# Performance work log

Measured on AMD Instinct MI355X. Metric: run time of the kernel, lower is better.

Reference implementation:

```python
import jax, jax.numpy as jnp
import numpy as np

SEQ = 4096
BLOCK = 64            # sparse_block_size
BLOCKS = SEQ // BLOCK # 64 block rows/cols
NUM_ORACLES = 32
ORACLE = SEQ // NUM_ORACLES      # 128
LOCAL_BLOCKS = ORACLE // BLOCK   # 2 (sliding-window width in blocks)
PATTERN_ID = 0


def _build_block_mask(pattern_id=PATTERN_ID):
    # Mirrors DKernelPredefinedSparseAttention.__init__ create_mask((i,))
    q_pos = np.arange(BLOCKS)[:, None]
    k_pos = np.arange(BLOCKS)[None, :]
    causal = q_pos >= k_pos
    sliding = (q_pos - k_pos) < LOCAL_BLOCKS
    vert = np.zeros(BLOCKS, dtype=bool)
    real_col = int(pattern_id * ORACLE + 0.5)
    cs = real_col // BLOCK
    ce = (real_col + ORACLE) // BLOCK
    vert[cs:ce] = True
    vert[0:1] = True  # global block 0 always visible
    return causal & (sliding | vert[None, :])


def setup_inputs() -> dict:
    key = jax.random.key(0)
    kq, kk, kv = jax.random.split(key, 3)
    shape = (1, SEQ, 8, 128)  # bshd, matches module's own smoke test layout
    q = jax.random.normal(kq, shape, dtype=jnp.float32)
    k = jax.random.normal(kk, shape, dtype=jnp.float32)
    v = jax.random.normal(kv, shape, dtype=jnp.float32)
    block_mask = jnp.asarray(_build_block_mask())  # [BLOCKS, BLOCKS] bool
    return {"q": q, "k": k, "v": v, "block_mask": block_mask}


def reference(q, k, v, block_mask):
    # Expand block-level mask to token level: [S, S]
    tok_mask = jnp.repeat(jnp.repeat(block_mask, BLOCK, axis=0), BLOCK, axis=1)
    scale = 1.0 / jnp.sqrt(jnp.asarray(q.shape[-1], q.dtype))
    # bshd x bshd -> bhqk scores
    scores = jnp.einsum("bqhd,bkhd->bhqk", q, k) * scale
    neg = jnp.asarray(-1e30, scores.dtype)
    scores = jnp.where(tok_mask[None, None, :, :], scores, neg)
    probs = jax.nn.softmax(scores, axis=-1)
    out = jnp.einsum("bhqk,bkhd->bqhd", probs, v)
    return out
```

## Files before the change

### kernel.cpp

```cpp
#include <hip/hip_runtime.h>
#include <hip/hip_bf16.h>

typedef __bf16 bf16x4 __attribute__((ext_vector_type(4)));
typedef __bf16 bf16x8 __attribute__((ext_vector_type(8)));
typedef short short4v __attribute__((ext_vector_type(4)));
typedef float floatx4 __attribute__((ext_vector_type(4)));

constexpr int SEQ = 4096;
constexpr int NH  = 8;
constexpr int DH  = 128;
constexpr int BLK = 64;
constexpr int QBLOCKS = SEQ / BLK;
constexpr int RS = NH * DH;
constexpr float SCALE = 0.088388347648318447f;
constexpr float MSHIFT = 8.0f;

#if __has_builtin(__builtin_amdgcn_mfma_f32_16x16x16_bf16)
  #define HAVE_PV16 1
  __device__ __forceinline__ floatx4 pv16(bf16x4 a, bf16x4 b, floatx4 c) {
      return __builtin_amdgcn_mfma_f32_16x16x16_bf16(a, b, c, 0, 0, 0);
  }
#elif __has_builtin(__builtin_amdgcn_mfma_f32_16x16x16bf16_1k)
  #define HAVE_PV16 1
  __device__ __forceinline__ floatx4 pv16(bf16x4 a, bf16x4 b, floatx4 c) {
      short4v as, bs;
      __builtin_memcpy(&as, &a, 8);
      __builtin_memcpy(&bs, &b, 8);
      return __builtin_amdgcn_mfma_f32_16x16x16bf16_1k(as, bs, c, 0, 0, 0);
  }
#else
  #define HAVE_PV16 0
#endif

__device__ __forceinline__ int calc_blist(int qb, int* blist) {
    int cand[4] = {0, 1, qb - 1, qb};
    int nb = 0;
    for (int i = 0; i < 4; ++i) {
        int b = cand[i];
        if (b < 0 || b > qb) continue;
        bool dup = false;
        for (int j = 0; j < nb; ++j) dup = dup || (blist[j] == b);
        if (!dup) blist[nb++] = b;
    }
    return nb;
}

__device__ __forceinline__ bf16x8 load8f(const float* p) {
    float4 a = *(const float4*)p;
    float4 b = *(const float4*)(p + 4);
    bf16x8 r = { (__bf16)a.x, (__bf16)a.y, (__bf16)a.z, (__bf16)a.w,
                 (__bf16)b.x, (__bf16)b.y, (__bf16)b.z, (__bf16)b.w };
    return r;
}

__global__ __launch_bounds__(1024, 4) void sparse_attn_kernel(
    const float* __restrict__ Q,
    const float* __restrict__ K,
    const float* __restrict__ V,
    float* __restrict__ Out)
{
    const int qb   = blockIdx.x;
    const int h    = blockIdx.y;
    const int tid  = threadIdx.x;
    const int wave = tid >> 6;
    const int g    = wave >> 2;
    const int ws   = wave & 3;
    const int lane = tid & 63;
    const int quad = lane >> 4;
    const int l16  = lane & 15;

    __shared__ __align__(16) __bf16 smem[4 * 8192];
    __bf16* vq    = smem + g * 8192;
    float*  l_arr = (float*)smem;

    int blist[4];
    const int nb = calc_blist(qb, blist);
    const bool valid = (g < nb);
    const int kb = valid ? blist[g] : 0;

    const int qrow = qb * BLK + ws * 16 + l16;
    const float* qp = Q + (size_t)qrow * RS + h * DH;
    bf16x8 qfrag[4];
#pragma unroll
    for (int sx = 0; sx < 4; ++sx)
        qfrag[sx] = load8f(qp + sx * 32 + quad * 8);

    const int tg   = tid & 255;
    const int dh   = tg & 127;
    const int kq   = tg >> 7;
    const int dht  = dh >> 4;
    const int l16v = dh & 15;
    if (valid) {
        const float* base = V + (size_t)(kb * BLK + kq * 32) * RS + h * DH + dh;
#if HAVE_PV16
#pragma unroll
        for (int n2 = 0; n2 < 2; ++n2) {
            const int n = kq * 2 + n2;
#pragma unroll
            for (int qv = 0; qv < 4; ++qv) {
                bf16x4 pk;
#pragma unroll
                for (int j = 0; j < 4; ++j)
                    pk[j] = (__bf16)base[(size_t)(n2 * 16 + qv * 4 + j) * RS];
                *(bf16x4*)(vq + ((n * 8 + dht) * 64 + qv * 16 + l16v) * 4) = pk;
            }
        }
#else
#pragma unroll
        for (int qv = 0; qv < 4; ++qv) {
            bf16x8 pk;
#pragma unroll
            for (int j = 0; j < 8; ++j)
                pk[j] = (__bf16)base[(size_t)(qv * 8 + j) * RS];
            *(bf16x8*)(vq + ((kq * 8 + dht) * 64 + qv * 16 + l16v) * 8) = pk;
        }
#endif
    }

    floatx4 sfragT[4];
    float lp = 0.f;
    if (valid) {
#pragma unroll
        for (int n = 0; n < 4; ++n) {
            floatx4 c = floatx4{0.f, 0.f, 0.f, 0.f};
            const float* kp =
                K + (size_t)(kb * BLK + n * 16 + l16) * RS + h * DH;
#pragma unroll
            for (int sx = 0; sx < 4; ++sx) {
                bf16x8 kf = load8f(kp + sx * 32 + quad * 8);
                c = __builtin_amdgcn_mfma_f32_16x16x32_bf16(kf, qfrag[sx], c, 0, 0, 0);
            }
            sfragT[n] = c;
        }
#pragma unroll
        for (int n = 0; n < 4; ++n)
#pragma unroll
            for (int r = 0; r < 4; ++r) {
                float p = __expf(fmaf(sfragT[n][r], SCALE, -MSHIFT));
                sfragT[n][r] = p;
                lp += p;
            }
        lp += __shfl_xor(lp, 16, 64);
        lp += __shfl_xor(lp, 32, 64);
    }

    __syncthreads();

    floatx4 o_acc[8];
#pragma unroll
    for (int n = 0; n < 8; ++n) o_acc[n] = floatx4{0.f, 0.f, 0.f, 0.f};
    if (valid) {
#if HAVE_PV16
        bf16x4 pa[4];
#pragma unroll
        for (int n = 0; n < 4; ++n) {
            bf16x4 t = { (__bf16)sfragT[n][0], (__bf16)sfragT[n][1],
                         (__bf16)sfragT[n][2], (__bf16)sfragT[n][3] };
            pa[n] = t;
        }
#pragma unroll
        for (int d = 0; d < 8; ++d)
#pragma unroll
            for (int n = 0; n < 4; ++n) {
                bf16x4 vb = *(const bf16x4*)(vq + ((n * 8 + d) * 64 + lane) * 4);
                o_acc[d] = pv16(pa[n], vb, o_acc[d]);
            }
#else
        bf16x8 pa8[2];
#pragma unroll
        for (int s2 = 0; s2 < 2; ++s2) {
            bf16x8 t;
#pragma unroll
            for (int jj = 0; jj < 8; ++jj) {
                const int srcl = ((quad & 1) * 2 + (jj >> 2)) * 16 + l16;
                float a = __shfl(sfragT[2 * s2][jj & 3], srcl, 64);
                float b = __shfl(sfragT[2 * s2 + 1][jj & 3], srcl, 64);
                t[jj] = (__bf16)((quad >> 1) ? b : a);
            }
            pa8[s2] = t;
        }
#pragma unroll
        for (int d = 0; d < 8; ++d)
#pragma unroll
            for (int s2 = 0; s2 < 2; ++s2) {
                bf16x8 vb = *(const bf16x8*)(vq + ((s2 * 8 + d) * 64 + lane) * 8);
                o_acc[d] = __builtin_amdgcn_mfma_f32_16x16x32_bf16(pa8[s2], vb, o_acc[d], 0, 0, 0);
            }
#endif
    }

    __syncthreads();

    if (valid) {
        if (g > 0) {
#pragma unroll
            for (int r = 0; r < 4; ++r) {
                const int row = ws * 16 + quad * 4 + r;
                bf16x8 w;
#pragma unroll
                for (int d = 0; d < 8; ++d) w[d] = (__bf16)o_acc[d][r];
                *(bf16x8*)(vq + row * 128 + l16 * 8) = w;
            }
        }
        if (quad == 0) l_arr[g * 64 + ws * 16 + l16] = lp;
    }
    __syncthreads();

    if (g == 0) {
#pragma unroll
        for (int r = 0; r < 4; ++r) {
            const int row = ws * 16 + quad * 4 + r;
            float l_tot = __shfl(lp, quad * 4 + r, 64);
            float os[8];
#pragma unroll
            for (int d = 0; d < 8; ++d) os[d] = o_acc[d][r];
            for (int gg = 1; gg < nb; ++gg) {
                l_tot += l_arr[gg * 64 + row];
                bf16x8 w = *(const bf16x8*)(smem + gg * 8192 + row * 128 + l16 * 8);
#pragma unroll
                for (int d = 0; d < 8; ++d) os[d] += (float)w[d];
            }
            const float inv = 1.f / l_tot;
            float* op = Out + (size_t)(qb * BLK + row) * RS + h * DH + l16;
#pragma unroll
            for (int d = 0; d < 8; ++d)
                op[d * 16] = os[d] * inv;
        }
    }
}

extern "C" void kernel_launch(void* const* d_in, const int* in_sizes, int n_in,
                              void* d_out, int out_size, void* d_ws, size_t ws_size,
                              hipStream_t stream) {
    const float* Q = (const float*)d_in[0];
    const float* K = (const float*)d_in[1];
    const float* V = (const float*)d_in[2];
    float* Out = (float*)d_out;

    dim3 grid(QBLOCKS, NH);
    sparse_attn_kernel<<<grid, 1024, 0, stream>>>(Q, K, V, Out);
}
```

Measured before the change: 141.9 us.

## Pre-pack Q/K/V to bf16 MFMA-friendly layout in a separate kernel

Adds a pack kernel that converts Q, K and V from fp32 to bf16 once, storing Q/K head-major and V pre-swizzled into the MFMA B-operand layout in workspace. The attention kernel then reads bf16 fragments straight from global memory, with no per-block fp32 conversion, no V staging through shared memory and one fewer barrier. Each K/V block is read by several query blocks, so converting once avoids redundant fp32 loads and conversions. The cost is a second kernel launch plus a round trip of the packed tensors through workspace memory.

```diff
diff --git a/kernel.cpp b/kernel.cpp
--- a/kernel.cpp
+++ b/kernel.cpp
@@ -14,6 +14,9 @@
 constexpr int RS = NH * DH;
 constexpr float SCALE = 0.088388347648318447f;
 constexpr float MSHIFT = 8.0f;
+
+constexpr size_t KP_OFF = (size_t)NH * SEQ * DH * 2;
+constexpr size_t VP_OFF = 2 * KP_OFF;
 
 #if __has_builtin(__builtin_amdgcn_mfma_f32_16x16x16_bf16)
   #define HAVE_PV16 1
@@ -53,10 +56,66 @@
     return r;
 }
 
-__global__ __launch_bounds__(1024, 4) void sparse_attn_kernel(
+__global__ __launch_bounds__(256) void pack_kernel(
     const float* __restrict__ Q,
     const float* __restrict__ K,
     const float* __restrict__ V,
+    __bf16* __restrict__ Qp,
+    __bf16* __restrict__ Kp,
+    __bf16* __restrict__ Vp)
+{
+    const int qb  = blockIdx.x;
+    const int h   = blockIdx.y;
+    const int z   = blockIdx.z;
+    const int tid = threadIdx.x;
+
+    if (z < 2) {
+        const float* src = (z == 0) ? Q : K;
+        __bf16* dst = (z == 0) ? Qp : Kp;
+        const int row = tid >> 2;
+        const int d0  = (tid & 3) * 32;
+        const float* ip = src + (size_t)(qb * BLK + row) * RS + h * DH + d0;
+        __bf16* op = dst + (size_t)(h * SEQ + qb * BLK + row) * DH + d0;
+#pragma unroll
+        for (int c = 0; c < 4; ++c)
+            *(bf16x8*)(op + c * 8) = load8f(ip + c * 8);
+    } else {
+        const int dh   = tid & 127;
+        const int kq   = tid >> 7;
+        const int dht  = dh >> 4;
+        const int l16v = dh & 15;
+        const float* base = V + (size_t)(qb * BLK + kq * 32) * RS + h * DH + dh;
+        __bf16* vt = Vp + (size_t)(h * QBLOCKS + qb) * 8192;
+#if HAVE_PV16
+#pragma unroll
+        for (int n2 = 0; n2 < 2; ++n2) {
+            const int n = kq * 2 + n2;
+#pragma unroll
+            for (int qv = 0; qv < 4; ++qv) {
+                bf16x4 pk;
+#pragma unroll
+                for (int j = 0; j < 4; ++j)
+                    pk[j] = (__bf16)base[(size_t)(n2 * 16 + qv * 4 + j) * RS];
+                *(bf16x4*)(vt + ((n * 8 + dht) * 64 + qv * 16 + l16v) * 4) = pk;
+            }
+        }
+#else
+#pragma unroll
+        for (int qv = 0; qv < 4; ++qv) {
+            bf16x8 pk;
+#pragma unroll
+            for (int j = 0; j < 8; ++j)
+                pk[j] = (__bf16)base[(size_t)(qv * 8 + j) * RS];
+            *(bf16x8*)(vt + ((kq * 8 + dht) * 64 + qv * 16 + l16v) * 8) = pk;
+        }
+#endif
+    }
+}
+
+__global__ __launch_bounds__(1024, 4) void attn_kernel(
+    const __bf16* __restrict__ Qp,
+    const __bf16* __restrict__ Kp,
+    const __bf16* __restrict__ Vp,
     float* __restrict__ Out)
 {
     const int qb   = blockIdx.x;
@@ -70,7 +129,7 @@
     const int l16  = lane & 15;
 
     __shared__ __align__(16) __bf16 smem[4 * 8192];
-    __bf16* vq    = smem + g * 8192;
+    __bf16* pq    = smem + g * 8192;
     float*  l_arr = (float*)smem;
 
     int blist[4];
@@ -78,44 +137,11 @@
     const bool valid = (g < nb);
     const int kb = valid ? blist[g] : 0;
 
-    const int qrow = qb * BLK + ws * 16 + l16;
-    const float* qp = Q + (size_t)qrow * RS + h * DH;
+    const __bf16* qp = Qp + (size_t)(h * SEQ + qb * BLK + ws * 16 + l16) * DH;
     bf16x8 qfrag[4];
 #pragma unroll
     for (int sx = 0; sx < 4; ++sx)
-        qfrag[sx] = load8f(qp + sx * 32 + quad * 8);
-
-    const int tg   = tid & 255;
-    const int dh   = tg & 127;
-    const int kq   = tg >> 7;
-    const int dht  = dh >> 4;
-    const int l16v = dh & 15;
-    if (valid) {
-        const float* base = V + (size_t)(kb * BLK + kq * 32) * RS + h * DH + dh;
-#if HAVE_PV16
-#pragma unroll
-        for (int n2 = 0; n2 < 2; ++n2) {
-            const int n = kq * 2 + n2;
-#pragma unroll
-            for (int qv = 0; qv < 4; ++qv) {
-                bf16x4 pk;
-#pragma unroll
-                for (int j = 0; j < 4; ++j)
-                    pk[j] = (__bf16)base[(size_t)(n2 * 16 + qv * 4 + j) * RS];
-                *(bf16x4*)(vq + ((n * 8 + dht) * 64 + qv * 16 + l16v) * 4) = pk;
-            }
-        }
-#else
-#pragma unroll
-        for (int qv = 0; qv < 4; ++qv) {
-            bf16x8 pk;
-#pragma unroll
-            for (int j = 0; j < 8; ++j)
-                pk[j] = (__bf16)base[(size_t)(qv * 8 + j) * RS];
-            *(bf16x8*)(vq + ((kq * 8 + dht) * 64 + qv * 16 + l16v) * 8) = pk;
-        }
-#endif
-    }
+        qfrag[sx] = *(const bf16x8*)(qp + sx * 32 + quad * 8);
 
     floatx4 sfragT[4];
     float lp = 0.f;
@@ -123,11 +149,11 @@
 #pragma unroll
         for (int n = 0; n < 4; ++n) {
             floatx4 c = floatx4{0.f, 0.f, 0.f, 0.f};
-            const float* kp =
-                K + (size_t)(kb * BLK + n * 16 + l16) * RS + h * DH;
+            const __bf16* kp =
+                Kp + (size_t)(h * SEQ + kb * BLK + n * 16 + l16) * DH;
 #pragma unroll
             for (int sx = 0; sx < 4; ++sx) {
-                bf16x8 kf = load8f(kp + sx * 32 + quad * 8);
+                bf16x8 kf = *(const bf16x8*)(kp + sx * 32 + quad * 8);
                 c = __builtin_amdgcn_mfma_f32_16x16x32_bf16(kf, qfrag[sx], c, 0, 0, 0);
             }
             sfragT[n] = c;
@@ -144,12 +170,11 @@
         lp += __shfl_xor(lp, 32, 64);
     }
 
-    __syncthreads();
-
     floatx4 o_acc[8];
 #pragma unroll
     for (int n = 0; n < 8; ++n) o_acc[n] = floatx4{0.f, 0.f, 0.f, 0.f};
     if (valid) {
+        const __bf16* vt = Vp + (size_t)(h * QBLOCKS + kb) * 8192;
 #if HAVE_PV16
         bf16x4 pa[4];
 #pragma unroll
@@ -162,7 +187,7 @@
         for (int d = 0; d < 8; ++d)
 #pragma unroll
             for (int n = 0; n < 4; ++n) {
-                bf16x4 vb = *(const bf16x4*)(vq + ((n * 8 + d) * 64 + lane) * 4);
+                bf16x4 vb = *(const bf16x4*)(vt + ((n * 8 + d) * 64 + lane) * 4);
                 o_acc[d] = pv16(pa[n], vb, o_acc[d]);
             }
 #else
@@ -183,7 +208,7 @@
         for (int d = 0; d < 8; ++d)
 #pragma unroll
             for (int s2 = 0; s2 < 2; ++s2) {
-                bf16x8 vb = *(const bf16x8*)(vq + ((s2 * 8 + d) * 64 + lane) * 8);
+                bf16x8 vb = *(const bf16x8*)(vt + ((s2 * 8 + d) * 64 + lane) * 8);
                 o_acc[d] = __builtin_amdgcn_mfma_f32_16x16x32_bf16(pa8[s2], vb, o_acc[d], 0, 0, 0);
             }
 #endif
@@ -199,7 +224,7 @@
                 bf16x8 w;
 #pragma unroll
                 for (int d = 0; d < 8; ++d) w[d] = (__bf16)o_acc[d][r];
-                *(bf16x8*)(vq + row * 128 + l16 * 8) = w;
+                *(bf16x8*)(pq + row * 128 + l16 * 8) = w;
             }
         }
         if (quad == 0) l_arr[g * 64 + ws * 16 + l16] = lp;
@@ -237,6 +262,10 @@
     const float* V = (const float*)d_in[2];
     float* Out = (float*)d_out;
 
-    dim3 grid(QBLOCKS, NH);
-    sparse_attn_kernel<<<grid, 1024, 0, stream>>>(Q, K, V, Out);
-}
+    __bf16* Qp = (__bf16*)d_ws;
+    __bf16* Kp = (__bf16*)((char*)d_ws + KP_OFF);
+    __bf16* Vp = (__bf16*)((char*)d_ws + VP_OFF);
+
+    pack_kernel<<<dim3(QBLOCKS, NH, 3), 256, 0, stream>>>(Q, K, V, Qp, Kp, Vp);
+    attn_kernel<<<dim3(QBLOCKS, NH), 1024, 0, stream>>>(Qp, Kp, Vp, Out);
+}
```

Measured after the change: 155.8 us. +9.8%, slower.
